# Kernel optimization log

Measured on AMD Instinct MI355X. Metric: run time of the kernel, lower is better.

## Reference

```python
import jax, jax.numpy as jnp
import numpy as np

ALPHA = 0.9
T = 809          # doc_len_limit hard-coded in fofe_tricontext_encoder
M = 16           # opt['max_len'] (cand_len_limit)
BN_EPS = 1e-5


def _cand_indices(T, M):
    # Enumeration order matches get_sample_index: outer over start s, inner over span.
    s_list, e_list = [], []
    for s in range(T):
        for span in range(min(M, T - s)):
            s_list.append(s)
            e_list.append(s + span)
    return np.asarray(s_list, np.int32), np.asarray(e_list, np.int32)

_S_IDX, _E_IDX = _cand_indices(T, M)          # [N_CANDS] = [12824]
_SPAN = (_E_IDX - _S_IDX).astype(np.int64)
# FOFE decay coefficient alpha^(e-s+1) for subtracting the prefix before the span
_COEF = (ALPHA ** (_SPAN + 1)).astype(np.float32)
# Lower-triangular FOFE prefix operator: A[t,k] = alpha^(t-k) for k<=t
_DIFF = np.subtract.outer(np.arange(T), np.arange(T))
_AFWD = np.where(_DIFF >= 0, ALPHA ** np.maximum(_DIFF, 0), 0.0).astype(np.float32)


def _bn(x, g, b, m, v):
    return (x - m) * jax.lax.rsqrt(v + BN_EPS) * g + b


def _forward(doc_emb, query_emb, W1, g1, b1, m1, v1, W2, g2, b2, m2, v2, W3):
    B, Tt, Dd = doc_emb.shape
    A = jnp.asarray(_AFWD)
    # forward FOFE prefixes F[t] = sum_{k<=t} alpha^(t-k) x[k]; inverse FOFE suffixes
    F = jnp.einsum('tk,bkd->btd', A, doc_emb)          # [B,T,Dd]
    R = jnp.einsum('tk,bkd->btd', A.T, doc_emb)        # [B,T,Dd]
    Fp = jnp.concatenate([jnp.zeros((B, 1, Dd), F.dtype), F], axis=1)   # Fp[:,s]=F[s-1]
    Rp = jnp.concatenate([R, jnp.zeros((B, 1, Dd), R.dtype)], axis=1)   # Rp[:,e+1]
    s_idx = jnp.asarray(_S_IDX)
    e_idx = jnp.asarray(_E_IDX)
    coef = jnp.asarray(_COEF)
    lctx = Fp[:, s_idx]                                 # left context excl cand
    cand = F[:, e_idx] - coef[None, :, None] * Fp[:, s_idx]  # FOFE of span [s,e]
    rctx = Rp[:, e_idx + 1]                             # right context excl cand
    doc_fofe = jnp.concatenate([lctx, cand, rctx], axis=-1)  # [B,N,3*Dd]
    # query FOFE (fofe_linear): z = sum_t alpha^(Lq-1-t) q[t]
    Lq = query_emb.shape[1]
    w = (ALPHA ** jnp.arange(Lq - 1, -1, -1, dtype=jnp.float32))
    qf = jnp.einsum('t,btd->bd', w, query_emb)          # [B,E]
    N = doc_fofe.shape[1]
    qf_b = jnp.broadcast_to(qf[:, None, :], (B, N, qf.shape[-1]))
    dq = jnp.concatenate([doc_fofe, qf_b], axis=-1)     # [B,N,3*Dd+E]
    x = dq.reshape(B * N, -1)
    h = jax.nn.relu(_bn(x @ W1.T, g1, b1, m1, v1))      # 1x1 conv == GEMM
    h = jax.nn.relu(_bn(h @ W2.T, g2, b2, m2, v2))
    out = (h @ W3.T).reshape(B, N, 2)                   # 2 class scores per candidate
    return out


def setup_inputs() -> dict:
    key = jax.random.key(0)
    ks = jax.random.split(key, 13)
    B, Lq, Dd, E = 4, 30, 304, 300
    Cin, H4, H2 = 3 * Dd + E, 1024, 512
    return {
        'doc_emb': jax.random.normal(ks[0], (B, T, Dd), jnp.float32),
        'query_emb': jax.random.normal(ks[1], (B, Lq, E), jnp.float32),
        'W1': jax.random.normal(ks[2], (H4, Cin), jnp.float32) / np.sqrt(Cin),
        'g1': jax.random.normal(ks[3], (H4,), jnp.float32),
        'b1': jax.random.normal(ks[4], (H4,), jnp.float32),
        'm1': jax.random.normal(ks[5], (H4,), jnp.float32),
        'v1': jax.random.uniform(ks[6], (H4,), jnp.float32),
        'W2': jax.random.normal(ks[7], (H2, H4), jnp.float32) / np.sqrt(H4),
        'g2': jax.random.normal(ks[8], (H2,), jnp.float32),
        'b2': jax.random.normal(ks[9], (H2,), jnp.float32),
        'm2': jax.random.normal(ks[10], (H2,), jnp.float32),
        'v2': jax.random.uniform(ks[11], (H2,), jnp.float32),
        'W3': jax.random.normal(ks[12], (2, H2), jnp.float32) / np.sqrt(H2),
    }


def reference(doc_emb, query_emb, W1, g1, b1, m1, v1, W2, g2, b2, m2, v2, W3):
    return _forward(doc_emb, query_emb, W1, g1, b1, m1, v1, W2, g2, b2, m2, v2, W3)
```

## Files before the change

kernel.cpp:

```cpp
#include <hip/hip_runtime.h>
#include <string.h>

#define T_LEN   809
#define DD      304
#define EE      300
#define LQ      30
#define NCAND   12824
#define NPAD    12928
#define CIN     1212
#define H1      1024
#define H2      512
#define BATCH   4
#define MROWS_F (BATCH * NPAD)
#define KS      320
#define TPAD    3328

#define MP_SCAN0   0
#define MP_W1      416
#define MP_W2      4256
#define MP_BIAS2   6304
#define MP_BASE    6306
#define MP_TOTAL   7330

__device__ __constant__ float c_coef[16] = {
  0.9f, 0.81f, 0.729f, 0.6561f, 0.59049f, 0.531441f, 0.4782969f, 0.43046721f,
  0.387420489f, 0.3486784401f, 0.31381059609f, 0.282429536481f,
  0.2541865828329f, 0.22876792454961f, 0.205891132094649f, 0.1853020188851841f
};

__device__ __forceinline__ unsigned short f2bf(float f) {
  unsigned int u = __float_as_uint(f);
  u += 0x7fffu + ((u >> 16) & 1u);
  return (unsigned short)(u >> 16);
}
__device__ __forceinline__ float bf2f(unsigned int h) {
  return __uint_as_float(h << 16);
}

typedef const __attribute__((address_space(1))) unsigned int GU32;
typedef __attribute__((address_space(3))) unsigned int LU32;
__device__ __forceinline__ void async16(const unsigned short* g, unsigned short* l) {
  __builtin_amdgcn_global_load_lds((GU32*)g, (LU32*)l, 16, 0, 0);
}

__global__ __launch_bounds__(256) void k_prep(const float* __restrict__ doc,
                                              const float* __restrict__ qe,
                                              const float* __restrict__ W1,
                                              const float* __restrict__ g1,
                                              const float* __restrict__ b1,
                                              const float* __restrict__ m1,
                                              const float* __restrict__ v1,
                                              const float* __restrict__ W2,
                                              const float* __restrict__ g2,
                                              const float* __restrict__ b2,
                                              const float* __restrict__ m2,
                                              const float* __restrict__ v2,
                                              unsigned short* __restrict__ Fz,
                                              unsigned short* __restrict__ Rz,
                                              unsigned short* __restrict__ Wlc,
                                              unsigned short* __restrict__ Wr,
                                              unsigned short* __restrict__ W2b,
                                              float* __restrict__ bias2,
                                              float* __restrict__ baseW)
{
  __shared__ float qs[EE];
  const int vb  = blockIdx.x;
  const int tid = threadIdx.x;

  if (vb < MP_W1) {
    const int dchunk = vb & 1;
    const int rest   = vb >> 1;
    const int tchunk = rest % 26;
    const int b      = (rest / 26) & 3;
    const int dir    = rest / 104;
    const int d  = dchunk * 256 + tid;
    const int t0 = tchunk * 32;
    if (dir == 0) {
      if (tchunk == 0 && d < KS) Fz[((size_t)b * 810) * KS + d] = 0;
      if (d >= DD) return;
      const float* db = doc + (size_t)b * T_LEN * DD + d;
      int start = t0 - 96; if (start < 0) start = 0;
      int end = t0 + 31; if (end > T_LEN - 1) end = T_LEN - 1;
      float s = 0.f;
      for (int t = start; t <= end; ++t) {
        s = fmaf(0.9f, s, db[(size_t)t * DD]);
        if (t >= t0) Fz[((size_t)b * 810 + 1 + t) * KS + d] = f2bf(s);
      }
    } else {
      if (tchunk == 0 && d < KS) Rz[((size_t)b * 810 + 809) * KS + d] = 0;
      if (d >= DD) return;
      const float* db = doc + (size_t)b * T_LEN * DD + d;
      int t1 = t0 + 31; if (t1 > T_LEN - 1) t1 = T_LEN - 1;
      int start = t1 + 96; if (start > T_LEN - 1) start = T_LEN - 1;
      float s = 0.f;
      for (int t = start; t >= t0; --t) {
        s = fmaf(0.9f, s, db[(size_t)t * DD]);
        if (t <= t1) Rz[((size_t)b * 810 + t) * KS + d] = f2bf(s);
      }
    }
  } else if (vb < MP_W2) {
    const int e = (vb - MP_W1) * 256 + tid;
    const int j = e / KS;
    const int k = e - j * KS;
    int jj, koff; unsigned short* dst; size_t idx;
    if (j < 1024)      { jj = j;        koff = k;       dst = Wlc; idx = (size_t)j * KS + k; }
    else if (j < 2048) { jj = j - 1024; koff = 304 + k; dst = Wlc; idx = (size_t)j * KS + k; }
    else               { jj = j - 2048; koff = 608 + k; dst = Wr;  idx = (size_t)(j - 2048) * KS + k; }
    float w = 0.f;
    if (k < 304) w = W1[(size_t)jj * CIN + koff] * g1[jj] * rsqrtf(v1[jj] + 1e-5f);
    dst[idx] = f2bf(w);
  } else if (vb < MP_BIAS2) {
    const int e = (vb - MP_W2) * 256 + tid;
    const int j = e >> 10;
    const int k = e & 1023;
    const float w = W2[(size_t)j * H1 + k] * g2[j] * rsqrtf(v2[j] + 1e-5f);
    W2b[(size_t)j * H1 + k] = f2bf(w);
  } else if (vb < MP_BASE) {
    const int i = (vb - MP_BIAS2) * 256 + tid;
    if (i < H2) {
      const float s = g2[i] * rsqrtf(v2[i] + 1e-5f);
      bias2[i] = b2[i] - m2[i] * s;
    }
  } else {
    const int flat = vb - MP_BASE;
    const int b  = flat >> 8;
    const int jg = flat & 255;
    const float* q = qe + (size_t)b * LQ * EE;
    for (int k = tid; k < EE; k += 256) {
      float s = 0.f;
      for (int t = 0; t < LQ; ++t) s = fmaf(s, 0.9f, q[(size_t)t * EE + k]);
      qs[k] = s;
    }
    __syncthreads();
    const int wv   = tid >> 6;
    const int lane = tid & 63;
    const int j = jg * 4 + wv;
    const float* w = W1 + (size_t)j * CIN + 912;
    float acc = 0.f;
    for (int k = lane; k < EE; k += 64) acc = fmaf(qs[k], w[k], acc);
    #pragma unroll
    for (int off = 32; off; off >>= 1) acc += __shfl_down(acc, off);
    if (lane == 0) {
      const float sc = g1[j] * rsqrtf(v1[j] + 1e-5f);
      baseW[(size_t)b * 2048 + j]        = b1[j] - m1[j] * sc + acc * sc;
      baseW[(size_t)b * 2048 + 1024 + j] = 0.f;
    }
  }
}

typedef __attribute__((ext_vector_type(8))) short frag8;
typedef __attribute__((ext_vector_type(4))) float f32x4;

#define GEMM_KLOOP(A_, B_, K_)                                                   \
  __shared__ __align__(16) unsigned short As[128 * 32];                          \
  __shared__ __align__(16) unsigned short Bs[128 * 32];                          \
  const int tid  = threadIdx.x;                                                  \
  const int lane = tid & 63;                                                     \
  const int wv   = tid >> 6;                                                     \
  const int wm   = wv & 1, wn = wv >> 1;                                         \
  const int lr = lane >> 2;                                                      \
  const int lc = lane & 3;                                                       \
  const int sc = lc ^ ((lr >> 1) & 3);                                           \
  const unsigned short* gA = A_ + ((size_t)bm * 128 + wv * 32 + lr) * K_ + sc * 8; \
  const unsigned short* gB = B_ + ((size_t)bn * 128 + wv * 32 + lr) * K_ + sc * 8; \
  const size_t row16 = (size_t)16 * K_;                                          \
  unsigned short* lA0 = &As[wv * 1024];                                          \
  unsigned short* lB0 = &Bs[wv * 1024];                                          \
  f32x4 acc[4][4];                                                               \
  _Pragma("unroll")                                                              \
  for (int i = 0; i < 4; ++i)                                                    \
    _Pragma("unroll")                                                            \
    for (int j = 0; j < 4; ++j) acc[i][j] = (f32x4){0.f, 0.f, 0.f, 0.f};         \
  const int arow = lane & 15;                                                    \
  const int pg   = (lane >> 4) ^ ((arow >> 1) & 3);                              \
  const int aoff = (wm * 64 + arow) * 32 + pg * 8;                               \
  const int boff = (wn * 64 + arow) * 32 + pg * 8;                               \
  for (int kc = 0; kc < K_; kc += 32) {                                          \
    __syncthreads();                                                             \
    async16(gA + kc,         lA0);                                               \
    async16(gA + kc + row16, lA0 + 512);                                         \
    async16(gB + kc,         lB0);                                               \
    async16(gB + kc + row16, lB0 + 512);                                         \
    __syncthreads();                                                             \
    frag8 a[4], b[4];                                                            \
    _Pragma("unroll")                                                            \
    for (int i = 0; i < 4; ++i) a[i] = *(const frag8*)&As[aoff + i * 512];       \
    _Pragma("unroll")                                                            \
    for (int i = 0; i < 4; ++i) b[i] = *(const frag8*)&Bs[boff + i * 512];       \
    _Pragma("unroll")                                                            \
    for (int i = 0; i < 4; ++i)                                                  \
      _Pragma("unroll")                                                          \
      for (int j = 0; j < 4; ++j)                                                \
        acc[i][j] = __builtin_amdgcn_mfma_f32_16x16x32_bf16(a[i], b[j], acc[i][j], 0, 0, 0); \
  }

__global__ __launch_bounds__(256, 4) void k_ugemm(const unsigned short* __restrict__ Fz,
                                                  const unsigned short* __restrict__ Wlc,
                                                  const unsigned short* __restrict__ Rz,
                                                  const unsigned short* __restrict__ Wr,
                                                  const float* __restrict__ baseW,
                                                  unsigned short* __restrict__ UF,
                                                  unsigned short* __restrict__ UR)
{
  int bx = blockIdx.x;
  const int isUF = (bx < 416);
  const unsigned short *Ap, *Bp; unsigned short* Cp; int bn, bm, Nout;
  if (isUF) { Ap = Fz; Bp = Wlc; Cp = UF; bn = bx & 15; bm = bx >> 4; Nout = 2048; }
  else { bx -= 416; Ap = Rz; Bp = Wr; Cp = UR; bn = bx & 7; bm = bx >> 3; Nout = 1024; }
  GEMM_KLOOP(Ap, Bp, KS)
  const int crow0 = bm * 128 + wm * 64 + ((lane >> 4) << 2);
  const int ccol0 = bn * 128 + wn * 64 + arow;
  #pragma unroll
  for (int i = 0; i < 4; ++i)
    #pragma unroll
    for (int j = 0; j < 4; ++j) {
      const int col = ccol0 + j * 16;
      #pragma unroll
      for (int r = 0; r < 4; ++r) {
        const int row = crow0 + i * 16 + r;
        float v = acc[i][j][r];
        if (isUF) {
          int bb = row / 810; if (bb > 3) bb = 3;
          v += baseW[(size_t)bb * 2048 + col];
        }
        Cp[(size_t)row * Nout + col] = f2bf(v);
      }
    }
}

__global__ __launch_bounds__(512) void k_combine(const unsigned short* __restrict__ UF,
                                                 const unsigned short* __restrict__ UR,
                                                 unsigned short* __restrict__ h1)
{
  __shared__ float s_ul[1024];
  __shared__ float s_ucs[1024];
  const int flat = (blockIdx.x & 7) * 405 + (blockIdx.x >> 3);
  if (flat >= BATCH * T_LEN) return;
  const int b = flat / T_LEN;
  const int s = flat - b * T_LEN;
  const int oct = threadIdx.x >> 6;
  const int t = threadIdx.x & 63;
  const size_t rs = (size_t)b * 810 + s;
  const int e0 = t * 16;

  {
    const unsigned int u = *(const unsigned int*)(UF + rs * 2048 + threadIdx.x * 2);
    const unsigned int c = *(const unsigned int*)(UF + rs * 2048 + 1024 + threadIdx.x * 2);
    s_ul[threadIdx.x * 2]      = bf2f(u & 0xffff);
    s_ul[threadIdx.x * 2 + 1]  = bf2f(u >> 16);
    s_ucs[threadIdx.x * 2]     = bf2f(c & 0xffff);
    s_ucs[threadIdx.x * 2 + 1] = bf2f(c >> 16);
  }
  __syncthreads();

  float ul[16], ucs[16];
  #pragma unroll
  for (int k = 0; k < 4; ++k) {
    const float4 a = *(const float4*)&s_ul[e0 + k * 4];
    const float4 c = *(const float4*)&s_ucs[e0 + k * 4];
    ul[4*k] = a.x; ul[4*k+1] = a.y; ul[4*k+2] = a.z; ul[4*k+3] = a.w;
    ucs[4*k] = c.x; ucs[4*k+1] = c.y; ucs[4*k+2] = c.z; ucs[4*k+3] = c.w;
  }

  const int nspan = min(16, T_LEN - s);
  int r0;
  if (s < 794) r0 = s * 16;
  else { const int d = s - 794; r0 = 12704 + 15 * d - (d * (d - 1)) / 2; }

  #pragma unroll
  for (int sp = 0; sp < 16; sp += 8) {
    const int row = sp + oct;
    if (row < nspan) {
      const size_t re = rs + row + 1;
      const uint4 e0v = *(const uint4*)(UF + re * 2048 + 1024 + e0);
      const uint4 e1v = *(const uint4*)(UF + re * 2048 + 1024 + e0 + 8);
      const uint4 r0v = *(const uint4*)(UR + re * 1024 + e0);
      const uint4 r1v = *(const uint4*)(UR + re * 1024 + e0 + 8);
      const float c = c_coef[row];
      const unsigned int* pe0 = (const unsigned int*)&e0v;
      const unsigned int* pe1 = (const unsigned int*)&e1v;
      const unsigned int* pr0 = (const unsigned int*)&r0v;
      const unsigned int* pr1 = (const unsigned int*)&r1v;
      unsigned int o[8];
      #pragma unroll
      for (int i = 0; i < 4; ++i) {
        float xlo = ul[2*i]   + bf2f(pe0[i] & 0xffff) - c * ucs[2*i]   + bf2f(pr0[i] & 0xffff);
        float xhi = ul[2*i+1] + bf2f(pe0[i] >> 16)    - c * ucs[2*i+1] + bf2f(pr0[i] >> 16);
        xlo = xlo > 0.f ? xlo : 0.f;
        xhi = xhi > 0.f ? xhi : 0.f;
        o[i] = (unsigned int)f2bf(xlo) | ((unsigned int)f2bf(xhi) << 16);
        float ylo = ul[8+2*i]   + bf2f(pe1[i] & 0xffff) - c * ucs[8+2*i]   + bf2f(pr1[i] & 0xffff);
        float yhi = ul[8+2*i+1] + bf2f(pe1[i] >> 16)    - c * ucs[8+2*i+1] + bf2f(pr1[i] >> 16);
        ylo = ylo > 0.f ? ylo : 0.f;
        yhi = yhi > 0.f ? yhi : 0.f;
        o[4 + i] = (unsigned int)f2bf(ylo) | ((unsigned int)f2bf(yhi) << 16);
      }
      unsigned short* dst = h1 + ((size_t)b * NPAD + r0 + row) * H1 + e0;
      *(uint4*)dst = *(const uint4*)&o[0];
      *(uint4*)(dst + 8) = *(const uint4*)&o[4];
    }
  }
}

#define NT_K   16
#define NITER  8

__global__ __launch_bounds__(512, 2) void k_gemm2x(const unsigned short* __restrict__ A,
                                                   const unsigned short* __restrict__ B,
                                                   const float* __restrict__ bias,
                                                   const float* __restrict__ W3,
                                                   float* __restrict__ P)
{
  __shared__ __align__(16) unsigned short L[65536];

  const int orig = blockIdx.x;
  const int xcd = orig & 7, cidx = orig >> 3;
  const int wg = (xcd < 4 ? xcd * 51 : 204 + (xcd - 4) * 50) + cidx;
  const int bm = wg >> 1, bn = wg & 1;

  const int tid  = threadIdx.x;
  const int w    = tid >> 6;
  const int lane = tid & 63;
  const int wr = w >> 2, wc = w & 3;
  const int arow = lane & 15;
  const int acol_sh = ((((lane >> 4) << 4) ^ ((arow & 8) << 2)) >> 1);

  const int cs   = tid ^ (((tid >> 5) & 1) << 1);
  const size_t srcOff = ((size_t)(cs >> 2) << 10) + (size_t)((cs & 3) << 3);
  const unsigned short* Ab = A + ((size_t)bm << 18) + srcOff;
  const unsigned short* Bb = B + ((size_t)bn << 18) + srcOff;
  unsigned short* ldsw = &L[w * 512];

  const int aBase = (wr * 64 + arow) * 32 + acol_sh;
  const int bBase = 16384 + (wc * 32 + arow) * 32 + acol_sh;

  f32x4 acc[2][2][4][2];
  #pragma unroll
  for (int qm = 0; qm < 2; ++qm)
    #pragma unroll
    for (int qn = 0; qn < 2; ++qn)
      #pragma unroll
      for (int i = 0; i < 4; ++i)
        #pragma unroll
        for (int j = 0; j < 2; ++j) acc[qm][qn][i][j] = (f32x4){0.f, 0.f, 0.f, 0.f};

#define STAGE(buf_, isB_, half_, kt_)                                                 \
  {                                                                                   \
    const unsigned short* s_ = (isB_ ? Bb : Ab) + (size_t)(half_) * 131072 + (kt_) * 64; \
    unsigned short* d_ = ldsw + (buf_) * 32768 + (isB_) * 16384 + (half_) * 8192;     \
    async16(s_,      d_);                                                             \
    async16(s_ + 32, d_ + 4096);                                                      \
  }

#define PHASE(q_, qm_, qn_, VMW_, ...)                                                \
  {                                                                                   \
    frag8 af[4][2], bf[2][2];                                                         \
    _Pragma("unroll")                                                                 \
    for (int ks = 0; ks < 2; ++ks) {                                                  \
      _Pragma("unroll")                                                               \
      for (int i = 0; i < 4; ++i)                                                     \
        af[i][ks] = *(const frag8*)&L[(q_)*32768 + (qm_)*8192 + ks*4096 + i*512 + aBase]; \
      _Pragma("unroll")                                                               \
      for (int j = 0; j < 2; ++j)                                                     \
        bf[j][ks] = *(const frag8*)&L[(q_)*32768 + (qn_)*8192 + ks*4096 + j*512 + bBase]; \
    }                                                                                 \
    __VA_ARGS__                                                                       \
    __builtin_amdgcn_sched_barrier(0);                                                \
    __builtin_amdgcn_s_barrier();                                                     \
    asm volatile("s_waitcnt lgkmcnt(0)" ::: "memory");                                \
    __builtin_amdgcn_sched_barrier(0);                                                \
    __builtin_amdgcn_s_setprio(1);                                                    \
    _Pragma("unroll")                                                                 \
    for (int ks = 0; ks < 2; ++ks)                                                    \
      _Pragma("unroll")                                                               \
      for (int i = 0; i < 4; ++i)                                                     \
        _Pragma("unroll")                                                             \
        for (int j = 0; j < 2; ++j)                                                   \
          acc[qm_][qn_][i][j] = __builtin_amdgcn_mfma_f32_16x16x32_bf16(              \
              af[i][ks], bf[j][ks], acc[qm_][qn_][i][j], 0, 0, 0);                    \
    __builtin_amdgcn_s_setprio(0);                                                    \
    VMW_;                                                                             \
    __builtin_amdgcn_s_barrier();                                                     \
    __builtin_amdgcn_sched_barrier(0);                                                \
  }

#define VM_PF()                                                                       \
  { if (pf) asm volatile("s_waitcnt vmcnt(4)" ::: "memory");                          \
    else    asm volatile("s_waitcnt vmcnt(0)" ::: "memory"); }
#define VM_NONE()

  STAGE(0, 0, 0, 0);
  STAGE(0, 1, 0, 0);
  STAGE(0, 0, 1, 0);
  STAGE(0, 1, 1, 0);
  STAGE(1, 0, 0, 1);
  STAGE(1, 1, 0, 1);
  asm volatile("s_waitcnt vmcnt(4)" ::: "memory");
  __builtin_amdgcn_s_barrier();
  __builtin_amdgcn_sched_barrier(0);

  for (int it = 0; it < NITER; ++it) {
    const int t = it * 2;
    const bool pf = (it < NITER - 1);
    PHASE(0, 0, 0, VM_NONE(), STAGE(1, 0, 1, t + 1);)
    PHASE(0, 0, 1, VM_NONE(), STAGE(1, 1, 1, t + 1);)
    PHASE(0, 1, 0, VM_NONE(), if (pf) STAGE(0, 0, 0, t + 2);)
    PHASE(0, 1, 1, VM_PF(),   if (pf) STAGE(0, 1, 0, t + 2);)
    PHASE(1, 0, 0, VM_NONE(), if (pf) STAGE(0, 0, 1, t + 2);)
    PHASE(1, 0, 1, VM_NONE(), if (pf) STAGE(0, 1, 1, t + 2);)
    PHASE(1, 1, 0, VM_NONE(), if (pf) STAGE(1, 0, 0, t + 3);)
    PHASE(1, 1, 1, VM_PF(),   if (pf) STAGE(1, 1, 0, t + 3);)
  }

  __syncthreads();
  float* redf = (float*)L;

  float bj[2][2], w0v[2][2], w1v[2][2];
  #pragma unroll
  for (int qn = 0; qn < 2; ++qn)
    #pragma unroll
    for (int j = 0; j < 2; ++j) {
      const int col = bn * 256 + qn * 128 + wc * 32 + j * 16 + arow;
      bj[qn][j]  = bias[col];
      w0v[qn][j] = W3[col];
      w1v[qn][j] = W3[H2 + col];
    }
  const int g = lane >> 4;
  #pragma unroll
  for (int qm = 0; qm < 2; ++qm)
    #pragma unroll
    for (int i = 0; i < 4; ++i)
      #pragma unroll
      for (int r = 0; r < 4; ++r) {
        float s0 = 0.f, s1 = 0.f;
        #pragma unroll
        for (int qn = 0; qn < 2; ++qn)
          #pragma unroll
          for (int j = 0; j < 2; ++j) {
            float v = acc[qm][qn][i][j][r] + bj[qn][j];
            v = v > 0.f ? v : 0.f;
            s0 = fmaf(v, w0v[qn][j], s0);
            s1 = fmaf(v, w1v[qn][j], s1);
          }
        #pragma unroll
        for (int m = 1; m < 16; m <<= 1) { s0 += __shfl_xor(s0, m); s1 += __shfl_xor(s1, m); }
        if (arow == 0) {
          const int rl = qm * 128 + wr * 64 + i * 16 + g * 4 + r;
          redf[(rl * 4 + wc) * 2]     = s0;
          redf[(rl * 4 + wc) * 2 + 1] = s1;
        }
      }
  __syncthreads();
  {
    const int rl = tid >> 1, s = tid & 1;
    const float v = redf[(rl * 4 + 0) * 2 + s] + redf[(rl * 4 + 1) * 2 + s]
                  + redf[(rl * 4 + 2) * 2 + s] + redf[(rl * 4 + 3) * 2 + s];
    P[((size_t)(bm * 256 + rl)) * 4 + bn * 2 + s] = v;
  }
#undef STAGE
#undef PHASE
#undef VM_PF
#undef VM_NONE
}

__global__ __launch_bounds__(256) void k_fin(const float* __restrict__ P, float* __restrict__ out)
{
  const int row = blockIdx.x * 256 + threadIdx.x;
  if (row >= MROWS_F) return;
  const int b = row / NPAD;
  const int rr = row - b * NPAD;
  if (rr >= NCAND) return;
  const float4 pa = ((const float4*)P)[row];
  float* o = out + ((size_t)b * NCAND + rr) * 2;
  o[0] = pa.x + pa.z;
  o[1] = pa.y + pa.w;
}

extern "C" void kernel_launch(void* const* d_in, const int* in_sizes, int n_in,
                              void* d_out, int out_size, void* d_ws, size_t ws_size,
                              hipStream_t stream)
{
  const float* doc = (const float*)d_in[0];
  const float* qe  = (const float*)d_in[1];
  const float* W1  = (const float*)d_in[2];
  const float* g1  = (const float*)d_in[3];
  const float* b1  = (const float*)d_in[4];
  const float* m1  = (const float*)d_in[5];
  const float* v1  = (const float*)d_in[6];
  const float* W2  = (const float*)d_in[7];
  const float* g2  = (const float*)d_in[8];
  const float* b2  = (const float*)d_in[9];
  const float* m2  = (const float*)d_in[10];
  const float* v2  = (const float*)d_in[11];
  const float* W3  = (const float*)d_in[12];
  float* out = (float*)d_out;

  char* ws = (char*)d_ws;
  size_t off = 0;
  auto alloc = [&](size_t bytes) -> void* {
    void* p = ws + off;
    off = (off + bytes + 255) & ~(size_t)255;
    return p;
  };
  unsigned short* Fz    = (unsigned short*)alloc((size_t)TPAD * KS * 2);
  unsigned short* Rz    = (unsigned short*)alloc((size_t)TPAD * KS * 2);
  unsigned short* Wlc   = (unsigned short*)alloc((size_t)2048 * KS * 2);
  unsigned short* Wr    = (unsigned short*)alloc((size_t)1024 * KS * 2);
  unsigned short* W2b   = (unsigned short*)alloc((size_t)H2 * H1 * 2);
  float*          bias2 = (float*)alloc((size_t)H2 * 4);
  float*          baseW = (float*)alloc((size_t)BATCH * 2048 * 4);
  unsigned short* UF    = (unsigned short*)alloc((size_t)TPAD * 2048 * 2);
  unsigned short* UR    = (unsigned short*)alloc((size_t)TPAD * 1024 * 2);
  unsigned short* h1    = (unsigned short*)alloc((size_t)MROWS_F * H1 * 2);
  float*          P     = (float*)alloc((size_t)MROWS_F * 4 * 4);
  (void)ws_size;

  k_prep<<<dim3(MP_TOTAL), 256, 0, stream>>>(doc, qe, W1, g1, b1, m1, v1,
                                             W2, g2, b2, m2, v2,
                                             Fz, Rz, Wlc, Wr, W2b, bias2, baseW);
  k_ugemm<<<dim3(416 + 208), 256, 0, stream>>>(Fz, Wlc, Rz, Wr, baseW, UF, UR);
  k_combine<<<dim3(8 * 405), 512, 0, stream>>>(UF, UR, h1);
  k_gemm2x<<<dim3(404), 512, 0, stream>>>(h1, W2b, bias2, W3, P);
  k_fin<<<dim3((MROWS_F + 255) / 256), 256, 0, stream>>>(P, out);
}
```

Before: 235.0 us.

## Reuse A/B register fragments across GEMM phases and deepen async prefetch

Restructures the 8-phase MFMA main loop so that A and B fragments loaded from LDS are held in registers and reused across quadrants, visiting the quadrants in a snake order (00,01,11,10). Two phases per buffer now skip LDS loads entirely, which cuts LDS read traffic. The prologue also issues one more stage up front, and the vmcnt wait threshold is raised so more global-to-LDS copies can stay in flight. The cost is higher register pressure from the persistent fragments and a more fragile ordering of stage writes against buffer reuse.

```diff
diff --git a/kernel.cpp b/kernel.cpp
--- a/kernel.cpp
+++ b/kernel.cpp
@@ -344,6 +344,9 @@
         #pragma unroll
         for (int j = 0; j < 2; ++j) acc[qm][qn][i][j] = (f32x4){0.f, 0.f, 0.f, 0.f};
 
+  frag8 af[4][2];
+  frag8 bf0[2][2], bf1[2][2];
+
 #define STAGE(buf_, isB_, half_, kt_)                                                 \
   {                                                                                   \
     const unsigned short* s_ = (isB_ ? Bb : Ab) + (size_t)(half_) * 131072 + (kt_) * 64; \
@@ -352,24 +355,21 @@
     async16(s_ + 32, d_ + 4096);                                                      \
   }
 
-#define PHASE(q_, qm_, qn_, VMW_, ...)                                                \
-  {                                                                                   \
-    frag8 af[4][2], bf[2][2];                                                         \
+#define LOAD_A(q_, qm_)                                                               \
     _Pragma("unroll")                                                                 \
-    for (int ks = 0; ks < 2; ++ks) {                                                  \
+    for (int ks = 0; ks < 2; ++ks)                                                    \
       _Pragma("unroll")                                                               \
       for (int i = 0; i < 4; ++i)                                                     \
-        af[i][ks] = *(const frag8*)&L[(q_)*32768 + (qm_)*8192 + ks*4096 + i*512 + aBase]; \
+        af[i][ks] = *(const frag8*)&L[(q_)*32768 + (qm_)*8192 + ks*4096 + i*512 + aBase];
+
+#define LOAD_B(q_, qn_, bf_)                                                          \
+    _Pragma("unroll")                                                                 \
+    for (int ks = 0; ks < 2; ++ks)                                                    \
       _Pragma("unroll")                                                               \
       for (int j = 0; j < 2; ++j)                                                     \
-        bf[j][ks] = *(const frag8*)&L[(q_)*32768 + (qn_)*8192 + ks*4096 + j*512 + bBase]; \
-    }                                                                                 \
-    __VA_ARGS__                                                                       \
-    __builtin_amdgcn_sched_barrier(0);                                                \
-    __builtin_amdgcn_s_barrier();                                                     \
-    asm volatile("s_waitcnt lgkmcnt(0)" ::: "memory");                                \
-    __builtin_amdgcn_sched_barrier(0);                                                \
-    __builtin_amdgcn_s_setprio(1);                                                    \
+        bf_[j][ks] = *(const frag8*)&L[(q_)*32768 + (qn_)*8192 + ks*4096 + j*512 + bBase];
+
+#define MMA(qm_, qn_, bf_)                                                            \
     _Pragma("unroll")                                                                 \
     for (int ks = 0; ks < 2; ++ks)                                                    \
       _Pragma("unroll")                                                               \
@@ -377,17 +377,27 @@
         _Pragma("unroll")                                                             \
         for (int j = 0; j < 2; ++j)                                                   \
           acc[qm_][qn_][i][j] = __builtin_amdgcn_mfma_f32_16x16x32_bf16(              \
-              af[i][ks], bf[j][ks], acc[qm_][qn_][i][j], 0, 0, 0);                    \
+              af[i][ks], bf_[j][ks], acc[qm_][qn_][i][j], 0, 0, 0);
+
+#define PHW(LOADS_, MMA_, STAGE_, VMW_)                                               \
+  {                                                                                   \
+    LOADS_                                                                            \
+    STAGE_                                                                            \
+    __builtin_amdgcn_sched_barrier(0);                                                \
+    __builtin_amdgcn_s_barrier();                                                     \
+    asm volatile("s_waitcnt lgkmcnt(0)" ::: "memory");                                \
+    __builtin_amdgcn_sched_barrier(0);                                                \
+    __builtin_amdgcn_s_setprio(1);                                                    \
+    MMA_                                                                              \
     __builtin_amdgcn_s_setprio(0);                                                    \
-    VMW_;                                                                             \
+    VMW_                                                                              \
     __builtin_amdgcn_s_barrier();                                                     \
     __builtin_amdgcn_sched_barrier(0);                                                \
   }
 
 #define VM_PF()                                                                       \
-  { if (pf) asm volatile("s_waitcnt vmcnt(4)" ::: "memory");                          \
+  { if (pf) asm volatile("s_waitcnt vmcnt(6)" ::: "memory");                          \
     else    asm volatile("s_waitcnt vmcnt(0)" ::: "memory"); }
-#define VM_NONE()
 
   STAGE(0, 0, 0, 0);
   STAGE(0, 1, 0, 0);
@@ -395,21 +405,22 @@
   STAGE(0, 1, 1, 0);
   STAGE(1, 0, 0, 1);
   STAGE(1, 1, 0, 1);
-  asm volatile("s_waitcnt vmcnt(4)" ::: "memory");
+  STAGE(1, 1, 1, 1);
+  asm volatile("s_waitcnt vmcnt(6)" ::: "memory");
   __builtin_amdgcn_s_barrier();
   __builtin_amdgcn_sched_barrier(0);
 
   for (int it = 0; it < NITER; ++it) {
     const int t = it * 2;
     const bool pf = (it < NITER - 1);
-    PHASE(0, 0, 0, VM_NONE(), STAGE(1, 0, 1, t + 1);)
-    PHASE(0, 0, 1, VM_NONE(), STAGE(1, 1, 1, t + 1);)
-    PHASE(0, 1, 0, VM_NONE(), if (pf) STAGE(0, 0, 0, t + 2);)
-    PHASE(0, 1, 1, VM_PF(),   if (pf) STAGE(0, 1, 0, t + 2);)
-    PHASE(1, 0, 0, VM_NONE(), if (pf) STAGE(0, 0, 1, t + 2);)
-    PHASE(1, 0, 1, VM_NONE(), if (pf) STAGE(0, 1, 1, t + 2);)
-    PHASE(1, 1, 0, VM_NONE(), if (pf) STAGE(1, 0, 0, t + 3);)
-    PHASE(1, 1, 1, VM_PF(),   if (pf) STAGE(1, 1, 0, t + 3);)
+    PHW(LOAD_A(0,0) LOAD_B(0,0,bf0), MMA(0,0,bf0), STAGE(1,0,1,t+1);,        )
+    PHW(LOAD_B(0,1,bf1),             MMA(0,1,bf1), if(pf) STAGE(0,0,0,t+2);, )
+    PHW(LOAD_A(0,1),                 MMA(1,1,bf1), if(pf) STAGE(0,1,0,t+2);, )
+    PHW(,                            MMA(1,0,bf0), if(pf) STAGE(0,1,1,t+2);, VM_PF();)
+    PHW(LOAD_A(1,0) LOAD_B(1,0,bf0), MMA(0,0,bf0), if(pf) STAGE(0,0,1,t+2);, )
+    PHW(LOAD_B(1,1,bf1),             MMA(0,1,bf1), if(pf) STAGE(1,0,0,t+3);, )
+    PHW(LOAD_A(1,1),                 MMA(1,1,bf1), if(pf) STAGE(1,1,0,t+3);, )
+    PHW(,                            MMA(1,0,bf0), if(pf) STAGE(1,1,1,t+3);, VM_PF();)
   }
 
   __syncthreads();
@@ -458,9 +469,11 @@
     P[((size_t)(bm * 256 + rl)) * 4 + bn * 2 + s] = v;
   }
 #undef STAGE
-#undef PHASE
+#undef LOAD_A
+#undef LOAD_B
+#undef MMA
+#undef PHW
 #undef VM_PF
-#undef VM_NONE
 }
 
 __global__ __launch_bounds__(256) void k_fin(const float* __restrict__ P, float* __restrict__ out)
```

Result: faster. 226.8 us (-3.5%).
